# Performance work log

Measured on AMD Instinct MI355X. Metric: run time of the kernel, lower is better.

Reference implementation:

```python
import jax, jax.numpy as jnp
import numpy as np

EMBED_DIM = 1024
NUM_HEADS = 16
HEAD_DIM = EMBED_DIM // NUM_HEADS
BSZ, SEQ = 2, 2048


def setup_inputs() -> dict:
    key = jax.random.key(0)
    ks = jax.random.split(key, 7)
    s = 0.02  # keep logits in a sane range
    return {
        "hidden_states": jax.random.normal(ks[0], (BSZ, SEQ, EMBED_DIM), jnp.float32),
        "attention_mask": jnp.zeros((1, 1, SEQ, SEQ), jnp.float32),
        "q_w": jax.random.normal(ks[1], (2 * EMBED_DIM, EMBED_DIM), jnp.float32) * s,
        "q_b": jnp.zeros((2 * EMBED_DIM,), jnp.float32),
        "k_w": jax.random.normal(ks[2], (EMBED_DIM, EMBED_DIM), jnp.float32) * s,
        "k_b": jnp.zeros((EMBED_DIM,), jnp.float32),
        "v_w": jax.random.normal(ks[3], (EMBED_DIM, EMBED_DIM), jnp.float32) * s,
        "v_b": jnp.zeros((EMBED_DIM,), jnp.float32),
        "o_w": jax.random.normal(ks[4], (EMBED_DIM, EMBED_DIM), jnp.float32) * s,
        "o_b": jnp.zeros((EMBED_DIM,), jnp.float32),
    }


def reference(hidden_states, attention_mask, q_w, q_b, k_w, k_b, v_w, v_b, o_w, o_b):
    bsz, seq, _ = hidden_states.shape
    h, d = NUM_HEADS, HEAD_DIM
    inv_sqrt_d = 1.0 / np.sqrt(d).astype(np.float32)

    qg = hidden_states @ q_w.T + q_b                      # [b, s, 2*h*d]
    q, gate_logits = jnp.split(qg, [h * d], axis=-1)       # elementwise gate
    k = hidden_states @ k_w.T + k_b
    v = hidden_states @ v_w.T + v_b

    q = q.reshape(bsz, seq, h, d).transpose(0, 2, 1, 3)    # [b, h, s, d]
    k = k.reshape(bsz, seq, h, d).transpose(0, 2, 1, 3)
    v = v.reshape(bsz, seq, h, d).transpose(0, 2, 1, 3)

    scores = jnp.einsum("bhqd,bhkd->bhqk", q, k) * inv_sqrt_d
    scores = scores + attention_mask
    weights = jax.nn.softmax(scores, axis=-1)
    attn = jnp.einsum("bhqk,bhkd->bhqd", weights, v)       # [b, h, s, d]

    gate = jax.nn.sigmoid(gate_logits.reshape(bsz, seq, h, d).transpose(0, 2, 1, 3))
    attn = attn * gate

    attn = attn.transpose(0, 2, 1, 3).reshape(bsz, seq, h * d)
    return attn @ o_w.T + o_b
```

## Files before the change

kernel.cpp:

```cpp
#include <hip/hip_runtime.h>
#include <cstdint>
#include <cstddef>

#define AS1 __attribute__((address_space(1)))
#define AS3 __attribute__((address_space(3)))

typedef __bf16 bf16x8 __attribute__((ext_vector_type(8)));
typedef __bf16 bf16x4 __attribute__((ext_vector_type(4)));
typedef float  f32x4  __attribute__((ext_vector_type(4)));
typedef float  f32x16 __attribute__((ext_vector_type(16)));
typedef unsigned int u32x4 __attribute__((ext_vector_type(4)));

#define MFMA_BF16(a, b, c) __builtin_amdgcn_mfma_f32_16x16x32_bf16((a), (b), (c), 0, 0, 0)
#define MFMA32(a, b, c)    __builtin_amdgcn_mfma_f32_32x32x16_bf16((a), (b), (c), 0, 0, 0)

__device__ __forceinline__ void gload16(const __bf16* g, __bf16* l) {
  __builtin_amdgcn_global_load_lds((AS1 void*)(uintptr_t)g, (AS3 void*)l, 16, 0, 0);
}

__device__ __forceinline__ unsigned int cvtpk_bf16(float lo, float hi) {
  unsigned int r;
  asm("v_cvt_pk_bf16_f32 %0, %1, %2" : "=v"(r) : "v"(lo), "v"(hi));
  return r;
}

__device__ __forceinline__ void permswap(unsigned int& a, unsigned int& b) {
  asm volatile("v_permlane32_swap_b32 %0, %1" : "+v"(a), "+v"(b));
}

__device__ __forceinline__ float exp2_fast(float x) {
  float r;
  asm("v_exp_f32 %0, %1" : "=v"(r) : "v"(x));
  return r;
}

#define LOG2E 1.4426950408889634f

__global__ void cvt_all_kernel(
    const float* __restrict__ hs, const float* __restrict__ qw, const float* __restrict__ kw,
    const float* __restrict__ vw, const float* __restrict__ ow,
    __bf16* __restrict__ Xb, __bf16* __restrict__ qwb, __bf16* __restrict__ kwb,
    __bf16* __restrict__ vwb, __bf16* __restrict__ owb,
    const unsigned long long* __restrict__ mask, int* __restrict__ flag)
{
  const int gid = blockIdx.x * blockDim.x + threadIdx.x;
  const int stride = gridDim.x * blockDim.x;
  for (int i = gid; i < 1179648; i += stride) {
    const float* s; __bf16* d; int o;
    if (i < 524288)       { s = hs; d = Xb;  o = i; }
    else if (i < 786432)  { s = qw; d = qwb; o = i - 524288; }
    else if (i < 917504)  { s = kw; d = kwb; o = i - 786432; }
    else if (i < 1048576) { s = vw; d = vwb; o = i - 917504; }
    else                  { s = ow; d = owb; o = i - 1048576; }
    const float4* p = (const float4*)(s + (size_t)o * 8);
    float4 a = p[0], b = p[1];
    bf16x8 v;
    v[0] = (__bf16)a.x; v[1] = (__bf16)a.y; v[2] = (__bf16)a.z; v[3] = (__bf16)a.w;
    v[4] = (__bf16)b.x; v[5] = (__bf16)b.y; v[6] = (__bf16)b.z; v[7] = (__bf16)b.w;
    *(bf16x8*)(d + (size_t)o * 8) = v;
  }
  bool nz = false;
  for (int i = gid; i < 2097152; i += stride) nz |= (mask[i] != 0ull);
  if (nz) atomicOr(flag, 1);
}

__global__ __launch_bounds__(512, 2) void proj_kernel(
    const __bf16* __restrict__ X,
    const __bf16* __restrict__ qw, const float* __restrict__ qb,
    const __bf16* __restrict__ kw, const float* __restrict__ kb,
    const __bf16* __restrict__ vw, const float* __restrict__ vb,
    __bf16* __restrict__ Qo, __bf16* __restrict__ Ko,
    __bf16* __restrict__ VTo, __bf16* __restrict__ Go)
{
  extern __shared__ char smem[];

  const int bid = blockIdx.x;
  const int jj = bid >> 3;
  const int ntile = (bid & 7) * 2 + (jj >> 4);
  const int mtile = jj & 15;
  const int m0 = mtile * 256, n0 = ntile * 256;

  const __bf16* W; const float* bias; int nb;
  if (n0 < 2048)      { W = qw; bias = qb; nb = n0; }
  else if (n0 < 3072) { W = kw; bias = kb; nb = n0 - 2048; }
  else                { W = vw; bias = vb; nb = n0 - 3072; }

  const int tid = threadIdx.x;
  const int wid = tid >> 6;
  const int wr = wid >> 2;
  const int wc = wid & 3;
  const int ln = tid & 63;
  const int qr = ln & 15, qg = ln >> 4;

  const int srow = ln >> 3;
  const int sgran = ((ln & 7) ^ srow) * 8;

#define SA(buf, half, kt) do { \
  _Pragma("unroll") for (int i_ = 0; i_ < 2; ++i_) { \
    const int r0_ = (half) * 64 + i_ * 128 + wid * 8; \
    gload16(X + (size_t)(m0 + r0_ + srow) * 1024 + (kt) * 64 + sgran, \
            (__bf16*)(smem + (buf) * 32768 + r0_ * 128)); \
  } } while (0)

#define SB(buf, half, kt) do { \
  _Pragma("unroll") for (int i_ = 0; i_ < 2; ++i_) { \
    const int g_ = wid + i_ * 8; \
    const int r0_ = (g_ >> 2) * 64 + (half) * 32 + (g_ & 3) * 8; \
    gload16(W + (size_t)(nb + r0_ + srow) * 1024 + (kt) * 64 + sgran, \
            (__bf16*)(smem + 65536 + (buf) * 32768 + r0_ * 128)); \
  } } while (0)

#define LDA(buf, mh, mi, kk) (*(const bf16x8*)(smem + (buf) * 32768 + \
    (wr * 128 + (mh) * 64 + (mi) * 16 + qr) * 128 + (((kk) * 64 + qg * 16) ^ ((qr & 7) << 4))))
#define LDB(buf, nh, ni, kk) (*(const bf16x8*)(smem + 65536 + (buf) * 32768 + \
    (wc * 64 + (nh) * 32 + (ni) * 16 + qr) * 128 + (((kk) * 64 + qg * 16) ^ ((qr & 7) << 4))))

  f32x4 acc[8][4];
#pragma unroll
  for (int m = 0; m < 8; ++m)
#pragma unroll
    for (int n = 0; n < 4; ++n) acc[m][n] = 0.f;

  bf16x8 af[4][2], b0f[2][2], b1f[2][2];

#define QUAD(mh, nh, BF) do { \
  asm volatile("s_waitcnt lgkmcnt(0)"); \
  __builtin_amdgcn_sched_barrier(0); \
  __builtin_amdgcn_s_setprio(1); \
  _Pragma("unroll") for (int mi_ = 0; mi_ < 4; ++mi_) \
    _Pragma("unroll") for (int ni_ = 0; ni_ < 2; ++ni_) { \
      acc[(mh)*4+mi_][(nh)*2+ni_] = MFMA_BF16(af[mi_][0], BF[ni_][0], acc[(mh)*4+mi_][(nh)*2+ni_]); \
      acc[(mh)*4+mi_][(nh)*2+ni_] = MFMA_BF16(af[mi_][1], BF[ni_][1], acc[(mh)*4+mi_][(nh)*2+ni_]); \
    } \
  __builtin_amdgcn_s_setprio(0); \
} while (0)

#define BAR() __builtin_amdgcn_s_barrier()

  SA(0, 0, 0); SA(0, 1, 0); SB(0, 0, 0); SB(0, 1, 0);
  SA(1, 0, 1); SB(1, 0, 1); SB(1, 1, 1);
  asm volatile("s_waitcnt vmcnt(6)");
  BAR();

  for (int it = 0; it < 8; ++it) {
    const int tb = 2 * it + 1;
    const int tc = (2 * it + 2 < 16) ? 2 * it + 2 : 15;
    const int td = (2 * it + 3 < 16) ? 2 * it + 3 : 15;

#pragma unroll
    for (int mi = 0; mi < 4; ++mi) { af[mi][0] = LDA(0, 0, mi, 0); af[mi][1] = LDA(0, 0, mi, 1); }
#pragma unroll
    for (int ni = 0; ni < 2; ++ni) { b0f[ni][0] = LDB(0, 0, ni, 0); b0f[ni][1] = LDB(0, 0, ni, 1); }
    SA(1, 1, tb);
    BAR();
    QUAD(0, 0, b0f);
    BAR();
#pragma unroll
    for (int ni = 0; ni < 2; ++ni) { b1f[ni][0] = LDB(0, 1, ni, 0); b1f[ni][1] = LDB(0, 1, ni, 1); }
    SA(0, 0, tc);
    BAR();
    QUAD(0, 1, b1f);
    BAR();
#pragma unroll
    for (int mi = 0; mi < 4; ++mi) { af[mi][0] = LDA(0, 1, mi, 0); af[mi][1] = LDA(0, 1, mi, 1); }
    SB(0, 0, tc);
    BAR();
    QUAD(1, 1, b1f);
    BAR();
    SB(0, 1, tc);
    asm volatile("s_waitcnt vmcnt(6)");
    BAR();
    QUAD(1, 0, b0f);
    BAR();

#pragma unroll
    for (int mi = 0; mi < 4; ++mi) { af[mi][0] = LDA(1, 0, mi, 0); af[mi][1] = LDA(1, 0, mi, 1); }
#pragma unroll
    for (int ni = 0; ni < 2; ++ni) { b0f[ni][0] = LDB(1, 0, ni, 0); b0f[ni][1] = LDB(1, 0, ni, 1); }
    SA(0, 1, tc);
    BAR();
    QUAD(0, 0, b0f);
    BAR();
#pragma unroll
    for (int ni = 0; ni < 2; ++ni) { b1f[ni][0] = LDB(1, 1, ni, 0); b1f[ni][1] = LDB(1, 1, ni, 1); }
    SA(1, 0, td);
    BAR();
    QUAD(0, 1, b1f);
    BAR();
#pragma unroll
    for (int mi = 0; mi < 4; ++mi) { af[mi][0] = LDA(1, 1, mi, 0); af[mi][1] = LDA(1, 1, mi, 1); }
    SB(1, 0, td);
    BAR();
    QUAD(1, 1, b1f);
    BAR();
    SB(1, 1, td);
    asm volatile("s_waitcnt vmcnt(6)");
    BAR();
    QUAD(1, 0, b0f);
    BAR();
  }

#pragma unroll
  for (int mi = 0; mi < 8; ++mi) {
    const int gm0 = m0 + wr * 128 + mi * 16 + qg * 4;
    const int b = gm0 >> 11;
    const int s = gm0 & 2047;
#pragma unroll
    for (int ni = 0; ni < 4; ++ni) {
      const int nl = wc * 64 + ni * 16 + qr;
      const float bb = bias[nb + nl];
      if (n0 < 1024) {
        const int col = n0 + nl, hh = col >> 6, dd = col & 63;
        __bf16* dst = Qo + ((size_t)((b << 4) + hh)) * 131072 + (size_t)s * 64 + dd;
#pragma unroll
        for (int rr = 0; rr < 4; ++rr) dst[(size_t)rr * 64] = (__bf16)((acc[mi][ni][rr] + bb) * (0.125f * LOG2E));
      } else if (n0 < 2048) {
        const int j = n0 - 1024 + nl;
        __bf16* dst = Go + (size_t)gm0 * 1024 + j;
#pragma unroll
        for (int rr = 0; rr < 4; ++rr) {
          const float v = acc[mi][ni][rr] + bb;
          dst[(size_t)rr * 1024] = (__bf16)(1.f / (1.f + __expf(-v)));
        }
      } else if (n0 < 3072) {
        const int j = n0 - 2048 + nl, hh = j >> 6, dd = j & 63;
        __bf16* dst = Ko + ((size_t)((b << 4) + hh)) * 131072 + (size_t)s * 64 + dd;
#pragma unroll
        for (int rr = 0; rr < 4; ++rr) dst[(size_t)rr * 64] = (__bf16)(acc[mi][ni][rr] + bb);
      } else {
        const int j = n0 - 3072 + nl, hh = j >> 6, dd = j & 63;
        bf16x4 pv;
#pragma unroll
        for (int rr = 0; rr < 4; ++rr) pv[rr] = (__bf16)(acc[mi][ni][rr] + bb);
        *(bf16x4*)(VTo + ((size_t)((b << 4) + hh)) * 131072 + (size_t)dd * 2048 + s) = pv;
      }
    }
  }
#undef SA
#undef SB
#undef LDA
#undef LDB
#undef QUAD
#undef BAR
}

__global__ __launch_bounds__(256, 2) void attn_kernel(
    const __bf16* __restrict__ Qb, const __bf16* __restrict__ Kb,
    const __bf16* __restrict__ VT, const __bf16* __restrict__ G,
    const float* __restrict__ mask, const int* __restrict__ flag,
    __bf16* __restrict__ attn)
{
  __shared__ __bf16 Ksh[2][32][128];
  __shared__ __bf16 Vsh[2][32][128];

  const int bid = blockIdx.x;
  const int y = bid >> 3;
  const int hl = (bid & 7) * 4 + (y >> 4);
  const int tid = threadIdx.x;
  const int w = tid >> 6;
  const int ln = tid & 63;
  const int lq = ln & 31;
  const int hi = ln >> 5;
  const int q0 = (y & 15) * 128 + w * 32;
  const int b = hl >> 4, h = hl & 15;

  const __bf16* Qh = Qb + (size_t)hl * 131072;
  const __bf16* Kh = Kb + (size_t)hl * 131072;
  const __bf16* Vh = VT + (size_t)hl * 131072;

  int kco[2], vco[2], ldst[2];
#pragma unroll
  for (int i = 0; i < 2; ++i) {
    const int prow = w * 8 + i * 4 + (ln >> 4);
    const int bphys = (ln & 15) * 16;
    const int blog = bphys ^ ((prow & 15) << 4);
    const int half = blog >> 7;
    const int col = (blog & 127) >> 1;
    kco[i] = (half * 32 + prow) * 64 + col;
    vco[i] = (half * 32 + prow) * 2048 + col;
    ldst[i] = (w * 8 + i * 4) * 256;
  }
  const int swz = (lq & 15) << 4;
  const int krow = lq * 256;

  bf16x8 qf[4];
#pragma unroll
  for (int ks = 0; ks < 4; ++ks)
    qf[ks] = *(const bf16x8*)(Qh + (size_t)(q0 + lq) * 64 + ks * 16 + hi * 8);

  f32x16 o0, o1;
#pragma unroll
  for (int i = 0; i < 16; ++i) { o0[i] = 0.f; o1[i] = 0.f; }
  float mrun = -1e30f, lrun = 0.f;

  const bool um = (*flag) != 0;

  char* Kc = (char*)&Ksh[0][0][0];  char* Kn = (char*)&Ksh[1][0][0];
  char* Vc = (char*)&Vsh[0][0][0];  char* Vn = (char*)&Vsh[1][0][0];

#pragma unroll
  for (int i = 0; i < 2; ++i) {
    gload16(Kh + kco[i], (__bf16*)(Kc + ldst[i]));
    gload16(Vh + vco[i], (__bf16*)(Vc + ldst[i]));
  }
  __syncthreads();

  for (int c = 0; c < 32; ++c) {
    const int kv0 = c * 64;
    if (c < 31) {
      const int kvn = kv0 + 64;
#pragma unroll
      for (int i = 0; i < 2; ++i) {
        gload16(Kh + kvn * 64 + kco[i], (__bf16*)(Kn + ldst[i]));
        gload16(Vh + kvn + vco[i],      (__bf16*)(Vn + ldst[i]));
      }
    }

    bf16x8 kfa[4], kfb[4];
#pragma unroll
    for (int ks = 0; ks < 4; ++ks) {
      kfa[ks] = *(const bf16x8*)(Kc + krow + ((ks * 32 + hi * 16) ^ swz));
      kfb[ks] = *(const bf16x8*)(Kc + krow + ((128 + ks * 32 + hi * 16) ^ swz));
    }
    f32x16 sa, sb;
#pragma unroll
    for (int i = 0; i < 16; ++i) { sa[i] = 0.f; sb[i] = 0.f; }
    __builtin_amdgcn_s_setprio(1);
#pragma unroll
    for (int ks = 0; ks < 4; ++ks) sa = MFMA32(kfa[ks], qf[ks], sa);
#pragma unroll
    for (int ks = 0; ks < 4; ++ks) sb = MFMA32(kfb[ks], qf[ks], sb);
    __builtin_amdgcn_s_setprio(0);

    float p[32];
    if (um) {
      const size_t mrow = (size_t)(q0 + lq) * 2048 + kv0;
#pragma unroll
      for (int i = 0; i < 16; ++i) {
        const int off = (i & 3) + 8 * (i >> 2) + 4 * hi;
        p[i]      = sa[i] + mask[mrow + off] * LOG2E;
        p[16 + i] = sb[i] + mask[mrow + 32 + off] * LOG2E;
      }
    } else {
#pragma unroll
      for (int i = 0; i < 16; ++i) { p[i] = sa[i]; p[16 + i] = sb[i]; }
    }

    float t = fmaxf(p[0], p[1]);
#pragma unroll
    for (int i = 2; i < 32; ++i) t = fmaxf(t, p[i]);
    t = fmaxf(t, __shfl_xor(t, 32));

    if (t > mrun + 8.f) {
      const float al = exp2_fast(mrun - t);
      mrun = t;
      lrun *= al;
#pragma unroll
      for (int i = 0; i < 16; ++i) { o0[i] *= al; o1[i] *= al; }
    }

    float ps = 0.f;
#pragma unroll
    for (int i = 0; i < 32; ++i) { p[i] = exp2_fast(p[i] - mrun); ps += p[i]; }
    lrun += ps;

    bf16x8 pa2[4];
#pragma unroll
    for (int g = 0; g < 4; ++g) {
      const int base = (g >> 1) * 16 + (g & 1) * 8;
      unsigned int c0 = cvtpk_bf16(p[base + 0], p[base + 1]);
      unsigned int c1 = cvtpk_bf16(p[base + 2], p[base + 3]);
      unsigned int c2 = cvtpk_bf16(p[base + 4], p[base + 5]);
      unsigned int c3 = cvtpk_bf16(p[base + 6], p[base + 7]);
      permswap(c0, c2);
      permswap(c1, c3);
      u32x4 wv; wv.x = c0; wv.y = c1; wv.z = c2; wv.w = c3;
      pa2[g] = __builtin_bit_cast(bf16x8, wv);
    }

    __builtin_amdgcn_s_setprio(1);
#pragma unroll
    for (int g = 0; g < 4; ++g) {
      const int kvb = (g >> 1) * 64 + (g & 1) * 32 + hi * 16;
      bf16x8 v0 = *(const bf16x8*)(Vc + krow + ((0 + kvb) ^ swz));
      bf16x8 v1 = *(const bf16x8*)(Vc + krow + ((128 + kvb) ^ swz));
      o0 = MFMA32(v0, pa2[g], o0);
      o1 = MFMA32(v1, pa2[g], o1);
    }
    __builtin_amdgcn_s_setprio(0);

    __syncthreads();
    char* tk = Kc; Kc = Kn; Kn = tk;
    char* tv = Vc; Vc = Vn; Vn = tv;
  }

  lrun += __shfl_xor(lrun, 32);
  const float inv = 1.f / lrun;
  const size_t base = ((size_t)(b * 2048 + q0 + lq)) * 1024 + h * 64;
#pragma unroll
  for (int half = 0; half < 2; ++half) {
#pragma unroll
    for (int g = 0; g < 4; ++g) {
      const int d0 = half * 32 + g * 8 + hi * 4;
      bf16x4 g4 = *(const bf16x4*)(G + base + d0);
      bf16x4 r4;
#pragma unroll
      for (int j = 0; j < 4; ++j) {
        const float ov = half ? o1[g * 4 + j] : o0[g * 4 + j];
        r4[j] = (__bf16)(ov * inv * (float)g4[j]);
      }
      *(bf16x4*)(attn + base + d0) = r4;
    }
  }
}

__global__ __launch_bounds__(256) void oproj_kernel(
    const __bf16* __restrict__ A, const __bf16* __restrict__ ow,
    const float* __restrict__ ob, float* __restrict__ C)
{
  __shared__ __bf16 As[2][128][64];
  __shared__ __bf16 Bs[2][128][64];
  const int bid = blockIdx.x;
  const int ntile = bid & 7;
  const int mtile = bid >> 3;
  const int m0 = mtile * 128, n0 = ntile * 128;

  const int tid = threadIdx.x;
  const int wv = tid >> 6, ln = tid & 63;
  const int wr = wv >> 1, wc = wv & 1;
  const int qr = ln & 15, qg = ln >> 4;
  const int lrow = ln >> 3, lcol = (ln & 7) * 8;

  f32x4 acc[4][4];
#pragma unroll
  for (int m = 0; m < 4; ++m)
#pragma unroll
    for (int n = 0; n < 4; ++n) acc[m][n] = 0.f;

  __bf16 (*Asc)[64] = As[0], (*Asn)[64] = As[1];
  __bf16 (*Bsc)[64] = Bs[0], (*Bsn)[64] = Bs[1];

#pragma unroll
  for (int i = 0; i < 4; ++i) {
    const int rb = i * 32 + wv * 8;
    gload16(A  + (size_t)(m0 + rb + lrow) * 1024 + lcol, &Asc[rb][0]);
    gload16(ow + (size_t)(n0 + rb + lrow) * 1024 + lcol, &Bsc[rb][0]);
  }
  __syncthreads();

  for (int t = 0; t < 16; ++t) {
    if (t < 15) {
      const int k0 = (t + 1) * 64;
#pragma unroll
      for (int i = 0; i < 4; ++i) {
        const int rb = i * 32 + wv * 8;
        gload16(A  + (size_t)(m0 + rb + lrow) * 1024 + k0 + lcol, &Asn[rb][0]);
        gload16(ow + (size_t)(n0 + rb + lrow) * 1024 + k0 + lcol, &Bsn[rb][0]);
      }
    }
#pragma unroll
    for (int kk = 0; kk < 2; ++kk) {
      bf16x8 af[4], bfv[4];
#pragma unroll
      for (int m = 0; m < 4; ++m) af[m] = *(const bf16x8*)&Asc[wr * 64 + m * 16 + qr][kk * 32 + qg * 8];
#pragma unroll
      for (int n = 0; n < 4; ++n) bfv[n] = *(const bf16x8*)&Bsc[wc * 64 + n * 16 + qr][kk * 32 + qg * 8];
#pragma unroll
      for (int m = 0; m < 4; ++m)
#pragma unroll
        for (int n = 0; n < 4; ++n) acc[m][n] = MFMA_BF16(af[m], bfv[n], acc[m][n]);
    }
    __syncthreads();
    __bf16 (*ta)[64] = Asc; Asc = Asn; Asn = ta;
    __bf16 (*tb)[64] = Bsc; Bsc = Bsn; Bsn = tb;
  }

#pragma unroll
  for (int m = 0; m < 4; ++m) {
    const int gm0 = m0 + wr * 64 + m * 16 + qg * 4;
#pragma unroll
    for (int n = 0; n < 4; ++n) {
      const int gn = n0 + wc * 64 + n * 16 + qr;
      const float bb = ob[gn];
      float* dst = C + (size_t)gm0 * 1024 + gn;
#pragma unroll
      for (int rr = 0; rr < 4; ++rr) dst[(size_t)rr * 1024] = acc[m][n][rr] + bb;
    }
  }
}

extern "C" void kernel_launch(void* const* d_in, const int* in_sizes, int n_in,
                              void* d_out, int out_size, void* d_ws, size_t ws_size,
                              hipStream_t stream)
{
  const float* hs   = (const float*)d_in[0];
  const float* mask = (const float*)d_in[1];
  const float* qw   = (const float*)d_in[2];
  const float* qb   = (const float*)d_in[3];
  const float* kw   = (const float*)d_in[4];
  const float* kb   = (const float*)d_in[5];
  const float* vw   = (const float*)d_in[6];
  const float* vb   = (const float*)d_in[7];
  const float* ow   = (const float*)d_in[8];
  const float* ob   = (const float*)d_in[9];
  float* out = (float*)d_out;

  char* w = (char*)d_ws;
  int*    flag = (int*)w;
  __bf16* Xb  = (__bf16*)(w + 256);
  __bf16* qwb = Xb  + 4194304;
  __bf16* kwb = qwb + 2097152;
  __bf16* vwb = kwb + 1048576;
  __bf16* owb = vwb + 1048576;
  __bf16* Qo  = owb + 1048576;
  __bf16* Ko  = Qo  + 4194304;
  __bf16* VTo = Ko  + 4194304;
  __bf16* Go  = VTo + 4194304;
  __bf16* At  = Go  + 4194304;

  hipFuncSetAttribute((const void*)proj_kernel, hipFuncAttributeMaxDynamicSharedMemorySize, 131072);

  hipMemsetAsync(flag, 0, sizeof(int), stream);
  cvt_all_kernel<<<2048, 256, 0, stream>>>(hs, qw, kw, vw, ow, Xb, qwb, kwb, vwb, owb,
                                           (const unsigned long long*)mask, flag);
  proj_kernel<<<256, 512, 131072, stream>>>(Xb, qwb, qb, kwb, kb, vwb, vb, Qo, Ko, VTo, Go);
  attn_kernel<<<512, 256, 0, stream>>>(Qo, Ko, VTo, Go, mask, flag, At);
  oproj_kernel<<<256, 256, 0, stream>>>(At, owb, ob, out);
}
```

Measured before the change: 138.5 us.

## Triple-buffer K/V tiles in attention kernel with two-chunk prefetch

Turns the K/V shared-memory double buffer into a three-slot ring buffer. Chunk c+2 is now fetched while chunk c is computed. The full __syncthreads is replaced by an explicit vmcnt wait plus a raw s_barrier, so only the next chunk's loads must finish before each iteration. Launch bounds are raised to 3 blocks per CU. The aim is to hide more global-load latency; in exchange the kernel uses 48KB of LDS per block and the occupancy hint adds register-pressure and spill risk.

```diff
diff --git a/kernel.cpp b/kernel.cpp
--- a/kernel.cpp
+++ b/kernel.cpp
@@ -244,14 +244,14 @@
 #undef BAR
 }
 
-__global__ __launch_bounds__(256, 2) void attn_kernel(
+__global__ __launch_bounds__(256, 3) void attn_kernel(
     const __bf16* __restrict__ Qb, const __bf16* __restrict__ Kb,
     const __bf16* __restrict__ VT, const __bf16* __restrict__ G,
     const float* __restrict__ mask, const int* __restrict__ flag,
     __bf16* __restrict__ attn)
 {
-  __shared__ __bf16 Ksh[2][32][128];
-  __shared__ __bf16 Vsh[2][32][128];
+  __shared__ __bf16 Ksh[3][32][128];
+  __shared__ __bf16 Vsh[3][32][128];
 
   const int bid = blockIdx.x;
   const int y = bid >> 3;
@@ -283,6 +283,13 @@
   const int swz = (lq & 15) << 4;
   const int krow = lq * 256;
 
+#define STAGE_AT(chunk, bb) do { \
+  const int kv0_ = (chunk) * 64; \
+  _Pragma("unroll") for (int i_ = 0; i_ < 2; ++i_) { \
+    gload16(Kh + kv0_ * 64 + kco[i_], (__bf16*)((char*)&Ksh[bb][0][0] + ldst[i_])); \
+    gload16(Vh + kv0_ + vco[i_],      (__bf16*)((char*)&Vsh[bb][0][0] + ldst[i_])); \
+  } } while (0)
+
   bf16x8 qf[4];
 #pragma unroll
   for (int ks = 0; ks < 4; ++ks)
@@ -295,26 +302,20 @@
 
   const bool um = (*flag) != 0;
 
-  char* Kc = (char*)&Ksh[0][0][0];  char* Kn = (char*)&Ksh[1][0][0];
-  char* Vc = (char*)&Vsh[0][0][0];  char* Vn = (char*)&Vsh[1][0][0];
-
-#pragma unroll
-  for (int i = 0; i < 2; ++i) {
-    gload16(Kh + kco[i], (__bf16*)(Kc + ldst[i]));
-    gload16(Vh + vco[i], (__bf16*)(Vc + ldst[i]));
-  }
-  __syncthreads();
-
+  STAGE_AT(0, 0);
+  STAGE_AT(1, 1);
+  asm volatile("s_waitcnt vmcnt(4)" ::: "memory");
+  __builtin_amdgcn_s_barrier();
+
+  int bufc = 0;
   for (int c = 0; c < 32; ++c) {
     const int kv0 = c * 64;
-    if (c < 31) {
-      const int kvn = kv0 + 64;
-#pragma unroll
-      for (int i = 0; i < 2; ++i) {
-        gload16(Kh + kvn * 64 + kco[i], (__bf16*)(Kn + ldst[i]));
-        gload16(Vh + kvn + vco[i],      (__bf16*)(Vn + ldst[i]));
-      }
-    }
+    if (c < 30) {
+      const int bnext = (bufc == 0) ? 2 : bufc - 1;
+      STAGE_AT(c + 2, bnext);
+    }
+    char* Kc = (char*)&Ksh[bufc][0][0];
+    char* Vc = (char*)&Vsh[bufc][0][0];
 
     bf16x8 kfa[4], kfb[4];
 #pragma unroll
@@ -389,10 +390,15 @@
     }
     __builtin_amdgcn_s_setprio(0);
 
-    __syncthreads();
-    char* tk = Kc; Kc = Kn; Kn = tk;
-    char* tv = Vc; Vc = Vn; Vn = tv;
-  }
+    if (c < 30) {
+      asm volatile("s_waitcnt vmcnt(4)" ::: "memory");
+    } else if (c == 30) {
+      asm volatile("s_waitcnt vmcnt(0)" ::: "memory");
+    }
+    if (c < 31) __builtin_amdgcn_s_barrier();
+    bufc = (bufc == 2) ? 0 : bufc + 1;
+  }
+#undef STAGE_AT
 
   lrun += __shfl_xor(lrun, 32);
   const float inv = 1.f / lrun;
```

Result: slower. 143.4 us (+3.5%).

## Process two KV chunks per barrier in attention loop with doubled LDS stages

Applied to the files above, without the earlier changes.

The attention kernel now stages two 64-key chunks per buffer, so each loop iteration handles 128 keys. It computes both QK^T score tiles up front, then runs softmax and PV for each sub-chunk. This halves the number of __syncthreads barriers and gives more independent MFMA work per load wait. In exchange, LDS use doubles to 64KB per block, which may limit the two-blocks-per-CU occupancy, and holding extra score accumulators raises register pressure.

```diff
diff --git a/kernel.cpp b/kernel.cpp
--- a/kernel.cpp
+++ b/kernel.cpp
@@ -250,8 +250,8 @@
     const float* __restrict__ mask, const int* __restrict__ flag,
     __bf16* __restrict__ attn)
 {
-  __shared__ __bf16 Ksh[2][32][128];
-  __shared__ __bf16 Vsh[2][32][128];
+  __shared__ __bf16 Ksh[2][2][32][128];
+  __shared__ __bf16 Vsh[2][2][32][128];
 
   const int bid = blockIdx.x;
   const int y = bid >> 3;
@@ -283,6 +283,18 @@
   const int swz = (lq & 15) << 4;
   const int krow = lq * 256;
 
+  char* const KB = (char*)&Ksh[0][0][0][0];
+  char* const VB = (char*)&Vsh[0][0][0][0];
+
+#define STAGE_SUB(chunk, bb, sb) do { \
+  const int kv0_ = (chunk) * 64; \
+  char* kd_ = KB + ((bb) * 2 + (sb)) * 8192; \
+  char* vd_ = VB + ((bb) * 2 + (sb)) * 8192; \
+  _Pragma("unroll") for (int i_ = 0; i_ < 2; ++i_) { \
+    gload16(Kh + kv0_ * 64 + kco[i_], (__bf16*)(kd_ + ldst[i_])); \
+    gload16(Vh + kv0_ + vco[i_],      (__bf16*)(vd_ + ldst[i_])); \
+  } } while (0)
+
   bf16x8 qf[4];
 #pragma unroll
   for (int ks = 0; ks < 4; ++ks)
@@ -295,104 +307,117 @@
 
   const bool um = (*flag) != 0;
 
-  char* Kc = (char*)&Ksh[0][0][0];  char* Kn = (char*)&Ksh[1][0][0];
-  char* Vc = (char*)&Vsh[0][0][0];  char* Vn = (char*)&Vsh[1][0][0];
-
-#pragma unroll
-  for (int i = 0; i < 2; ++i) {
-    gload16(Kh + kco[i], (__bf16*)(Kc + ldst[i]));
-    gload16(Vh + vco[i], (__bf16*)(Vc + ldst[i]));
-  }
+  STAGE_SUB(0, 0, 0);
+  STAGE_SUB(1, 0, 1);
   __syncthreads();
 
-  for (int c = 0; c < 32; ++c) {
-    const int kv0 = c * 64;
-    if (c < 31) {
-      const int kvn = kv0 + 64;
-#pragma unroll
-      for (int i = 0; i < 2; ++i) {
-        gload16(Kh + kvn * 64 + kco[i], (__bf16*)(Kn + ldst[i]));
-        gload16(Vh + kvn + vco[i],      (__bf16*)(Vn + ldst[i]));
-      }
-    }
-
-    bf16x8 kfa[4], kfb[4];
-#pragma unroll
-    for (int ks = 0; ks < 4; ++ks) {
-      kfa[ks] = *(const bf16x8*)(Kc + krow + ((ks * 32 + hi * 16) ^ swz));
-      kfb[ks] = *(const bf16x8*)(Kc + krow + ((128 + ks * 32 + hi * 16) ^ swz));
-    }
-    f32x16 sa, sb;
-#pragma unroll
-    for (int i = 0; i < 16; ++i) { sa[i] = 0.f; sb[i] = 0.f; }
-    __builtin_amdgcn_s_setprio(1);
-#pragma unroll
-    for (int ks = 0; ks < 4; ++ks) sa = MFMA32(kfa[ks], qf[ks], sa);
-#pragma unroll
-    for (int ks = 0; ks < 4; ++ks) sb = MFMA32(kfb[ks], qf[ks], sb);
-    __builtin_amdgcn_s_setprio(0);
-
-    float p[32];
-    if (um) {
-      const size_t mrow = (size_t)(q0 + lq) * 2048 + kv0;
-#pragma unroll
-      for (int i = 0; i < 16; ++i) {
-        const int off = (i & 3) + 8 * (i >> 2) + 4 * hi;
-        p[i]      = sa[i] + mask[mrow + off] * LOG2E;
-        p[16 + i] = sb[i] + mask[mrow + 32 + off] * LOG2E;
-      }
-    } else {
-#pragma unroll
-      for (int i = 0; i < 16; ++i) { p[i] = sa[i]; p[16 + i] = sb[i]; }
-    }
-
-    float t = fmaxf(p[0], p[1]);
-#pragma unroll
-    for (int i = 2; i < 32; ++i) t = fmaxf(t, p[i]);
-    t = fmaxf(t, __shfl_xor(t, 32));
-
-    if (t > mrun + 8.f) {
-      const float al = exp2_fast(mrun - t);
-      mrun = t;
-      lrun *= al;
-#pragma unroll
-      for (int i = 0; i < 16; ++i) { o0[i] *= al; o1[i] *= al; }
-    }
-
-    float ps = 0.f;
-#pragma unroll
-    for (int i = 0; i < 32; ++i) { p[i] = exp2_fast(p[i] - mrun); ps += p[i]; }
-    lrun += ps;
-
-    bf16x8 pa2[4];
-#pragma unroll
-    for (int g = 0; g < 4; ++g) {
-      const int base = (g >> 1) * 16 + (g & 1) * 8;
-      unsigned int c0 = cvtpk_bf16(p[base + 0], p[base + 1]);
-      unsigned int c1 = cvtpk_bf16(p[base + 2], p[base + 3]);
-      unsigned int c2 = cvtpk_bf16(p[base + 4], p[base + 5]);
-      unsigned int c3 = cvtpk_bf16(p[base + 6], p[base + 7]);
-      permswap(c0, c2);
-      permswap(c1, c3);
-      u32x4 wv; wv.x = c0; wv.y = c1; wv.z = c2; wv.w = c3;
-      pa2[g] = __builtin_bit_cast(bf16x8, wv);
-    }
-
-    __builtin_amdgcn_s_setprio(1);
-#pragma unroll
-    for (int g = 0; g < 4; ++g) {
-      const int kvb = (g >> 1) * 64 + (g & 1) * 32 + hi * 16;
-      bf16x8 v0 = *(const bf16x8*)(Vc + krow + ((0 + kvb) ^ swz));
-      bf16x8 v1 = *(const bf16x8*)(Vc + krow + ((128 + kvb) ^ swz));
-      o0 = MFMA32(v0, pa2[g], o0);
-      o1 = MFMA32(v1, pa2[g], o1);
-    }
-    __builtin_amdgcn_s_setprio(0);
+  int buf = 0;
+  for (int t = 0; t < 16; ++t) {
+    if (t < 15) {
+      STAGE_SUB(2 * t + 2, buf ^ 1, 0);
+      STAGE_SUB(2 * t + 3, buf ^ 1, 1);
+    }
+
+    f32x16 s0a, s0b, s1a, s1b;
+#pragma unroll
+    for (int i = 0; i < 16; ++i) { s0a[i] = 0.f; s0b[i] = 0.f; s1a[i] = 0.f; s1b[i] = 0.f; }
+    {
+      char* Kc0 = KB + (buf * 2 + 0) * 8192;
+      char* Kc1 = KB + (buf * 2 + 1) * 8192;
+      bf16x8 kfa[4], kfb[4];
+#pragma unroll
+      for (int ks = 0; ks < 4; ++ks) {
+        kfa[ks] = *(const bf16x8*)(Kc0 + krow + ((ks * 32 + hi * 16) ^ swz));
+        kfb[ks] = *(const bf16x8*)(Kc0 + krow + ((128 + ks * 32 + hi * 16) ^ swz));
+      }
+      __builtin_amdgcn_s_setprio(1);
+#pragma unroll
+      for (int ks = 0; ks < 4; ++ks) s0a = MFMA32(kfa[ks], qf[ks], s0a);
+#pragma unroll
+      for (int ks = 0; ks < 4; ++ks) s0b = MFMA32(kfb[ks], qf[ks], s0b);
+      __builtin_amdgcn_s_setprio(0);
+#pragma unroll
+      for (int ks = 0; ks < 4; ++ks) {
+        kfa[ks] = *(const bf16x8*)(Kc1 + krow + ((ks * 32 + hi * 16) ^ swz));
+        kfb[ks] = *(const bf16x8*)(Kc1 + krow + ((128 + ks * 32 + hi * 16) ^ swz));
+      }
+      __builtin_amdgcn_s_setprio(1);
+#pragma unroll
+      for (int ks = 0; ks < 4; ++ks) s1a = MFMA32(kfa[ks], qf[ks], s1a);
+#pragma unroll
+      for (int ks = 0; ks < 4; ++ks) s1b = MFMA32(kfb[ks], qf[ks], s1b);
+      __builtin_amdgcn_s_setprio(0);
+    }
+
+#pragma unroll
+    for (int sub = 0; sub < 2; ++sub) {
+      const int kv0 = (2 * t + sub) * 64;
+      char* Vc = VB + (buf * 2 + sub) * 8192;
+      f32x16& sA = sub ? s1a : s0a;
+      f32x16& sB = sub ? s1b : s0b;
+
+      float p[32];
+      if (um) {
+        const size_t mrow = (size_t)(q0 + lq) * 2048 + kv0;
+#pragma unroll
+        for (int i = 0; i < 16; ++i) {
+          const int off = (i & 3) + 8 * (i >> 2) + 4 * hi;
+          p[i]      = sA[i] + mask[mrow + off] * LOG2E;
+          p[16 + i] = sB[i] + mask[mrow + 32 + off] * LOG2E;
+        }
+      } else {
+#pragma unroll
+        for (int i = 0; i < 16; ++i) { p[i] = sA[i]; p[16 + i] = sB[i]; }
+      }
+
+      float tmx = fmaxf(p[0], p[1]);
+#pragma unroll
+      for (int i = 2; i < 32; ++i) tmx = fmaxf(tmx, p[i]);
+      tmx = fmaxf(tmx, __shfl_xor(tmx, 32));
+
+      if (tmx > mrun + 8.f) {
+        const float al = exp2_fast(mrun - tmx);
+        mrun = tmx;
+        lrun *= al;
+#pragma unroll
+        for (int i = 0; i < 16; ++i) { o0[i] *= al; o1[i] *= al; }
+      }
+
+      float ps = 0.f;
+#pragma unroll
+      for (int i = 0; i < 32; ++i) { p[i] = exp2_fast(p[i] - mrun); ps += p[i]; }
+      lrun += ps;
+
+      bf16x8 pa2[4];
+#pragma unroll
+      for (int g = 0; g < 4; ++g) {
+        const int base = (g >> 1) * 16 + (g & 1) * 8;
+        unsigned int c0 = cvtpk_bf16(p[base + 0], p[base + 1]);
+        unsigned int c1 = cvtpk_bf16(p[base + 2], p[base + 3]);
+        unsigned int c2 = cvtpk_bf16(p[base + 4], p[base + 5]);
+        unsigned int c3 = cvtpk_bf16(p[base + 6], p[base + 7]);
+        permswap(c0, c2);
+        permswap(c1, c3);
+        u32x4 wv; wv.x = c0; wv.y = c1; wv.z = c2; wv.w = c3;
+        pa2[g] = __builtin_bit_cast(bf16x8, wv);
+      }
+
+      __builtin_amdgcn_s_setprio(1);
+#pragma unroll
+      for (int g = 0; g < 4; ++g) {
+        const int kvb = (g >> 1) * 64 + (g & 1) * 32 + hi * 16;
+        bf16x8 v0 = *(const bf16x8*)(Vc + krow + ((0 + kvb) ^ swz));
+        bf16x8 v1 = *(const bf16x8*)(Vc + krow + ((128 + kvb) ^ swz));
+        o0 = MFMA32(v0, pa2[g], o0);
+        o1 = MFMA32(v1, pa2[g], o1);
+      }
+      __builtin_amdgcn_s_setprio(0);
+    }
 
     __syncthreads();
-    char* tk = Kc; Kc = Kn; Kn = tk;
-    char* tv = Vc; Vc = Vn; Vn = tv;
-  }
+    buf ^= 1;
+  }
+#undef STAGE_SUB
 
   lrun += __shfl_xor(lrun, 32);
   const float inv = 1.f / lrun;
```

Measured after the change: 137.9 us. Within noise of the previous version (-0.4%).
